# Optimization experiments

Measured on AMD Instinct MI355X. Metric: run time of the kernel, lower is better.

## Reference

```python
import jax, jax.numpy as jnp
import numpy as np

N_NODES = 100000
N_EDGES = 1600000
D = 128

def setup_inputs() -> dict:
    key = jax.random.key(0)
    ks = jax.random.split(key, 8)
    s = 1.0 / np.sqrt(D)
    x = jax.random.normal(ks[0], (N_NODES, D), dtype=jnp.float32)
    edge_index = jax.random.randint(ks[1], (2, N_EDGES), 0, N_NODES, dtype=jnp.int64)
    Wl1 = jax.random.normal(ks[2], (D, D), dtype=jnp.float32) * s
    Wr1 = jax.random.normal(ks[3], (D, D), dtype=jnp.float32) * s
    b1 = jax.random.normal(ks[4], (D,), dtype=jnp.float32) * s
    Wl2 = jax.random.normal(ks[5], (D, D), dtype=jnp.float32) * s
    Wr2 = jax.random.normal(ks[6], (D, D), dtype=jnp.float32) * s
    b2 = jax.random.normal(ks[7], (D,), dtype=jnp.float32) * s
    return {"x": x, "edge_index": edge_index, "Wl1": Wl1, "Wr1": Wr1, "b1": b1,
            "Wl2": Wl2, "Wr2": Wr2, "b2": b2}

def _sage_mean(x, src, dst, n, Wl, Wr, b):
    # mean-aggregate neighbor features onto destination nodes
    msg = x[src]                                      # [E, D] gather
    agg = jax.ops.segment_sum(msg, dst, num_segments=n)  # [N, D] scatter-add
    deg = jax.ops.segment_sum(jnp.ones((src.shape[0],), x.dtype), dst, num_segments=n)
    mean = agg / jnp.maximum(deg, 1.0)[:, None]
    # SAGEConv: lin_l(aggregated) + lin_r(self), bias on lin_l
    return mean @ Wl.T + x @ Wr.T + b

def reference(x, edge_index, Wl1, Wr1, b1, Wl2, Wr2, b2):
    src, dst = edge_index[0], edge_index[1]
    n = x.shape[0]
    h = _sage_mean(x, src, dst, n, Wl1, Wr1, b1)
    h = jax.nn.relu(h)
    return _sage_mean(h, src, dst, n, Wl2, Wr2, b2)
```

## Files before the change

### kernel.cpp

```cpp
#include <hip/hip_runtime.h>
#include <hip/hip_bf16.h>

#define NN 100000
#define NE 1600000
#define DD 128

#define ASHIFT 8
#define NSPAN  256
#define BK     391
#define BCAP   4608
#define EPB    4096
#define NAB    391
#define TFB    3125

typedef __attribute__((ext_vector_type(8))) short bf16x8;
typedef __attribute__((ext_vector_type(4))) float f32x4;
typedef __attribute__((ext_vector_type(2))) float f32x2;

__device__ inline unsigned short f2bf(float f) {
    unsigned u = __builtin_bit_cast(unsigned, f);
    u += 0x7fff + ((u >> 16) & 1);
    return (unsigned short)(u >> 16);
}
__device__ inline float bf2f(unsigned short h) {
    return __builtin_bit_cast(float, (unsigned)h << 16);
}

__global__ __launch_bounds__(512) void fusedA(const int* __restrict__ src,
                                              const int* __restrict__ dst,
                                              int* __restrict__ gcur,
                                              int* __restrict__ pairs,
                                              const float* __restrict__ in,
                                              unsigned short* __restrict__ outb,
                                              unsigned char* __restrict__ out8) {
    __shared__ int hist[BK];
    __shared__ int gbase[BK];
    __shared__ int lcur[BK];
    const int t = threadIdx.x;

    if (blockIdx.x >= NAB) {
        const size_t i = (size_t)(blockIdx.x - NAB) * 512 + t;
        const float4 a = *(const float4*)&in[i * 8];
        const float4 b = *(const float4*)&in[i * 8 + 4];
        unsigned short o[8] = {f2bf(a.x), f2bf(a.y), f2bf(a.z), f2bf(a.w),
                               f2bf(b.x), f2bf(b.y), f2bf(b.z), f2bf(b.w)};
        *(bf16x8*)&outb[i * 8] = *(bf16x8*)o;
        unsigned e0 = 0, e1 = 0;
        e0 = __builtin_amdgcn_cvt_pk_fp8_f32(a.x, a.y, e0, false);
        e0 = __builtin_amdgcn_cvt_pk_fp8_f32(a.z, a.w, e0, true);
        e1 = __builtin_amdgcn_cvt_pk_fp8_f32(b.x, b.y, e1, false);
        e1 = __builtin_amdgcn_cvt_pk_fp8_f32(b.z, b.w, e1, true);
        uint2 p = {e0, e1};
        *(uint2*)&out8[i * 8] = p;
        return;
    }

    const int e0 = blockIdx.x * EPB;

    for (int i = t; i < BK; i += 512) hist[i] = 0;
    __syncthreads();
    for (int i = t; i < EPB; i += 512) {
        int e = e0 + i;
        if (e < NE) atomicAdd(&hist[dst[e] >> ASHIFT], 1);
    }
    __syncthreads();
    for (int i = t; i < BK; i += 512) {
        int c = hist[i];
        gbase[i] = i * BCAP + (c ? atomicAdd(&gcur[i], c) : 0);
        lcur[i] = 0;
    }
    __syncthreads();
    for (int i = t; i < EPB; i += 512) {
        int e = e0 + i;
        if (e < NE) {
            int d = dst[e];
            int b = d >> ASHIFT;
            int r = atomicAdd(&lcur[b], 1);
            pairs[gbase[b] + r] = ((d & (NSPAN - 1)) << 17) | src[e];
        }
    }
}

__global__ __launch_bounds__(512) void bucketB(const int* __restrict__ pairs,
                                               const int* __restrict__ gcur,
                                               int* __restrict__ cnt,
                                               int* __restrict__ rowoff,
                                               int* __restrict__ csr) {
    __shared__ int bs[512];
    __shared__ int hist[NSPAN];
    __shared__ int scanbuf[NSPAN];
    const int b = blockIdx.x, t = threadIdx.x;

    int v = (t < BK) ? gcur[t] : 0;
    bs[t] = v;
    __syncthreads();
    #pragma unroll
    for (int d = 1; d < 512; d <<= 1) {
        int u = (t >= d) ? bs[t - d] : 0;
        __syncthreads();
        bs[t] += u;
        __syncthreads();
    }
    const int sz   = gcur[b];
    const int base = bs[b] - sz;

    const int n0    = b << ASHIFT;
    const int nodeN = min(NSPAN, NN - n0);
    const int* ep   = &pairs[(size_t)b * BCAP];

    for (int i = t; i < NSPAN; i += 512) hist[i] = 0;
    __syncthreads();
    for (int i = t; i < sz; i += 512) atomicAdd(&hist[((unsigned)ep[i]) >> 17], 1);
    __syncthreads();
    for (int i = t; i < nodeN; i += 512) cnt[n0 + i] = hist[i];
    for (int i = t; i < NSPAN; i += 512) scanbuf[i] = hist[i];
    __syncthreads();
    #pragma unroll
    for (int d = 1; d < NSPAN; d <<= 1) {
        int v0 = (t >= d && t < NSPAN) ? scanbuf[t - d] : 0;
        __syncthreads();
        if (t < NSPAN) scanbuf[t] += v0;
        __syncthreads();
    }
    for (int i = t; i < NSPAN; i += 512) {
        int excl = scanbuf[i] - hist[i];
        if (i < nodeN) rowoff[n0 + i] = base + excl;
        hist[i] = excl;
    }
    if (b == BK - 1 && t == 0) rowoff[NN] = NE;
    __syncthreads();
    for (int i = t; i < sz; i += 512) {
        int p = ep[i];
        int r = atomicAdd(&hist[((unsigned)p) >> 17], 1);
        csr[base + r] = p & 0x1FFFF;
    }
}

__global__ __launch_bounds__(256) void prepw(const float* __restrict__ Wl1,
                                             const float* __restrict__ Wr1,
                                             const float* __restrict__ Wl2,
                                             const float* __restrict__ Wr2,
                                             unsigned short* __restrict__ wsb) {
    const int tid = blockIdx.x * 256 + threadIdx.x;
    const int mat = tid >> 11;
    const int ko  = (tid >> 7) & 15;
    const int j   = tid & 127;
    const float* W = (mat == 0) ? Wl1 : (mat == 1) ? Wr1 : (mat == 2) ? Wl2 : Wr2;
    const float4 w0 = *(const float4*)&W[(size_t)j * DD + ko * 8];
    const float4 w1 = *(const float4*)&W[(size_t)j * DD + ko * 8 + 4];
    unsigned short o[8] = {f2bf(w0.x), f2bf(w0.y), f2bf(w0.z), f2bf(w0.w),
                           f2bf(w1.x), f2bf(w1.y), f2bf(w1.z), f2bf(w1.w)};
    *(bf16x8*)&wsb[(size_t)tid * 8] = *(bf16x8*)o;
}

__device__ inline void accum8(float* a, uint2 u) {
    f32x2 p;
    p = __builtin_amdgcn_cvt_pk_f32_fp8(u.x, false); a[0] += p.x; a[1] += p.y;
    p = __builtin_amdgcn_cvt_pk_f32_fp8(u.x, true);  a[2] += p.x; a[3] += p.y;
    p = __builtin_amdgcn_cvt_pk_f32_fp8(u.y, false); a[4] += p.x; a[5] += p.y;
    p = __builtin_amdgcn_cvt_pk_f32_fp8(u.y, true);  a[6] += p.x; a[7] += p.y;
}

__global__ __launch_bounds__(256) void gather_fp8(const unsigned char* __restrict__ feat,
                                                  const int* __restrict__ rowoff,
                                                  const int* __restrict__ csr,
                                                  const int* __restrict__ cnt,
                                                  unsigned short* __restrict__ mean) {
    const int node = blockIdx.x * 16 + (threadIdx.x >> 4);
    const int l8 = (threadIdx.x & 15) * 8;
    const int beg = rowoff[node], end = rowoff[node + 1];
    float a0[8] = {0, 0, 0, 0, 0, 0, 0, 0};
    float a1[8] = {0, 0, 0, 0, 0, 0, 0, 0};
    int j = beg;
    for (; j + 7 < end; j += 8) {
        int s0 = csr[j],     s1 = csr[j + 1], s2 = csr[j + 2], s3 = csr[j + 3];
        int s4 = csr[j + 4], s5 = csr[j + 5], s6 = csr[j + 6], s7 = csr[j + 7];
        uint2 u0 = *(const uint2*)&feat[(size_t)s0 * DD + l8];
        uint2 u1 = *(const uint2*)&feat[(size_t)s1 * DD + l8];
        uint2 u2 = *(const uint2*)&feat[(size_t)s2 * DD + l8];
        uint2 u3 = *(const uint2*)&feat[(size_t)s3 * DD + l8];
        uint2 u4 = *(const uint2*)&feat[(size_t)s4 * DD + l8];
        uint2 u5 = *(const uint2*)&feat[(size_t)s5 * DD + l8];
        uint2 u6 = *(const uint2*)&feat[(size_t)s6 * DD + l8];
        uint2 u7 = *(const uint2*)&feat[(size_t)s7 * DD + l8];
        accum8(a0, u0); accum8(a1, u1); accum8(a0, u2); accum8(a1, u3);
        accum8(a0, u4); accum8(a1, u5); accum8(a0, u6); accum8(a1, u7);
    }
    for (; j + 3 < end; j += 4) {
        int s0 = csr[j], s1 = csr[j + 1], s2 = csr[j + 2], s3 = csr[j + 3];
        uint2 u0 = *(const uint2*)&feat[(size_t)s0 * DD + l8];
        uint2 u1 = *(const uint2*)&feat[(size_t)s1 * DD + l8];
        uint2 u2 = *(const uint2*)&feat[(size_t)s2 * DD + l8];
        uint2 u3 = *(const uint2*)&feat[(size_t)s3 * DD + l8];
        accum8(a0, u0); accum8(a1, u1); accum8(a0, u2); accum8(a1, u3);
    }
    for (; j < end; ++j) {
        int s0 = csr[j];
        uint2 u0 = *(const uint2*)&feat[(size_t)s0 * DD + l8];
        accum8(a0, u0);
    }
    const float inv = 1.0f / fmaxf((float)cnt[node], 1.0f);
    unsigned short o[8];
    #pragma unroll
    for (int i = 0; i < 8; ++i) o[i] = f2bf((a0[i] + a1[i]) * inv);
    *(bf16x8*)&mean[(size_t)node * DD + l8] = *(bf16x8*)o;
}

__global__ __launch_bounds__(256, 3) void combine_mfma(
    const unsigned short* __restrict__ mean, const unsigned short* __restrict__ self,
    const unsigned short* __restrict__ wsb,
    const float* __restrict__ bias, void* __restrict__ outp,
    unsigned char* __restrict__ out8,
    int out_bf16, int do_relu)
{
    const int t = threadIdx.x;
    const int wv = t >> 6, lane = t & 63;
    const int m = lane & 15;
    const int q = lane >> 4;
    const int j0 = wv * 2;

    bf16x8 bfr[2][4][2];
    #pragma unroll
    for (int h = 0; h < 2; ++h)
        #pragma unroll
        for (int kq = 0; kq < 4; ++kq)
            #pragma unroll
            for (int jj = 0; jj < 2; ++jj)
                bfr[h][kq][jj] = *(const bf16x8*)
                    &wsb[((size_t)((h * 16 + kq * 4 + q) * 128) + (j0 + jj) * 16 + m) * 8];

    float bv[2];
    #pragma unroll
    for (int jj = 0; jj < 2; ++jj) bv[jj] = bias[(j0 + jj) * 16 + m];

    for (int tile = blockIdx.x; tile < NN / 16; tile += gridDim.x) {
        const size_t arow = ((size_t)tile * 16 + m) * DD;
        f32x4 acc[2];
        acc[0] = (f32x4){0.f, 0.f, 0.f, 0.f};
        acc[1] = (f32x4){0.f, 0.f, 0.f, 0.f};

        #pragma unroll
        for (int kq = 0; kq < 4; ++kq) {
            const bf16x8 am = *(const bf16x8*)&mean[arow + kq * 32 + q * 8];
            const bf16x8 as = *(const bf16x8*)&self[arow + kq * 32 + q * 8];
            #pragma unroll
            for (int jj = 0; jj < 2; ++jj) {
                acc[jj] = __builtin_amdgcn_mfma_f32_16x16x32_bf16(am, bfr[0][kq][jj], acc[jj], 0, 0, 0);
                acc[jj] = __builtin_amdgcn_mfma_f32_16x16x32_bf16(as, bfr[1][kq][jj], acc[jj], 0, 0, 0);
            }
        }

        #pragma unroll
        for (int jj = 0; jj < 2; ++jj) {
            const int col = (j0 + jj) * 16 + m;
            #pragma unroll
            for (int r = 0; r < 4; ++r) {
                const size_t row = (size_t)tile * 16 + q * 4 + r;
                float v = acc[jj][r] + bv[jj];
                if (do_relu) v = fmaxf(v, 0.0f);
                if (out_bf16)
                    ((unsigned short*)outp)[row * DD + col] = f2bf(v);
                else
                    ((float*)outp)[row * DD + col] = v;
                if (out8) {
                    unsigned p = __builtin_amdgcn_cvt_pk_fp8_f32(v, v, 0u, false);
                    out8[row * DD + col] = (unsigned char)p;
                }
            }
        }
    }
}

extern "C" void kernel_launch(void* const* d_in, const int* in_sizes, int n_in,
                              void* d_out, int out_size, void* d_ws, size_t ws_size,
                              hipStream_t stream) {
    const float* x   = (const float*)d_in[0];
    const int*   ei  = (const int*)d_in[1];
    const float* Wl1 = (const float*)d_in[2];
    const float* Wr1 = (const float*)d_in[3];
    const float* b1  = (const float*)d_in[4];
    const float* Wl2 = (const float*)d_in[5];
    const float* Wr2 = (const float*)d_in[6];
    const float* b2  = (const float*)d_in[7];
    const int* src = ei;
    const int* dst = ei + NE;
    float* out = (float*)d_out;

    unsigned short* xb   = (unsigned short*)d_ws;
    unsigned short* mean = xb + (size_t)NN * DD;
    unsigned short* h    = mean + (size_t)NN * DD;
    unsigned char*  x8   = (unsigned char*)(h + (size_t)NN * DD);
    unsigned char*  h8   = x8 + (size_t)NN * DD;
    int*  pairs  = (int*)(h8 + (size_t)NN * DD);
    int*  gcur   = pairs + (size_t)BK * BCAP;
    int*  cnt    = gcur + BK;
    int*  rowoff = cnt + NN;
    int*  csr    = rowoff + NN + 1;
    uintptr_t wp = ((uintptr_t)(csr + NE) + 255) & ~(uintptr_t)255;
    unsigned short* wsb = (unsigned short*)wp;

    hipMemsetAsync(gcur, 0, BK * sizeof(int), stream);
    prepw<<<32, 256, 0, stream>>>(Wl1, Wr1, Wl2, Wr2, wsb);
    fusedA<<<NAB + TFB, 512, 0, stream>>>(src, dst, gcur, pairs, x, xb, x8);
    bucketB<<<BK, 512, 0, stream>>>(pairs, gcur, cnt, rowoff, csr);

    gather_fp8<<<NN / 16, 256, 0, stream>>>(x8, rowoff, csr, cnt, mean);
    combine_mfma<<<2048, 256, 0, stream>>>(mean, xb, wsb, b1, h, h8, 1, 1);

    gather_fp8<<<NN / 16, 256, 0, stream>>>(h8, rowoff, csr, cnt, mean);
    combine_mfma<<<2048, 256, 0, stream>>>(mean, h, wsb + 32768, b2, out, nullptr, 0, 0);
}
```

Measured before the change: 289.5 us.

## Replace two-pass bucketed CSR build with global-atomic degree count and scatter

Drops the bucket-then-sort CSR construction, which staged edges through a pairs buffer and ran a local per-bucket sort. It is replaced by three passes: global atomic degree counting (fused with the bf16/fp8 conversion of x), a per-block scan that claims its base offset from a global atomic counter, and a scatter that places each edge using global atomics. Node segments no longer follow node order because block bases are taken in arrival order, so gather now uses rowoff plus cnt instead of rowoff[n+1]. This removes the pairs buffer traffic at the cost of heavy global atomic contention and a CSR order that is no longer deterministic.

```diff
diff --git a/kernel.cpp b/kernel.cpp
--- a/kernel.cpp
+++ b/kernel.cpp
@@ -5,13 +5,10 @@
 #define NE 1600000
 #define DD 128
 
-#define ASHIFT 8
-#define NSPAN  256
-#define BK     391
-#define BCAP   4608
-#define EPB    4096
-#define NAB    391
-#define TFB    3125
+#define DEGB 782
+#define TFB  3125
+#define SCT  782
+#define MKB  196
 
 typedef __attribute__((ext_vector_type(8))) short bf16x8;
 typedef __attribute__((ext_vector_type(4))) float f32x4;
@@ -26,20 +23,15 @@
     return __builtin_bit_cast(float, (unsigned)h << 16);
 }
 
-__global__ __launch_bounds__(512) void fusedA(const int* __restrict__ src,
-                                              const int* __restrict__ dst,
-                                              int* __restrict__ gcur,
-                                              int* __restrict__ pairs,
-                                              const float* __restrict__ in,
-                                              unsigned short* __restrict__ outb,
-                                              unsigned char* __restrict__ out8) {
-    __shared__ int hist[BK];
-    __shared__ int gbase[BK];
-    __shared__ int lcur[BK];
+__global__ __launch_bounds__(512) void fusedAdeg(const int* __restrict__ dst,
+                                                 int* __restrict__ cnt,
+                                                 const float* __restrict__ in,
+                                                 unsigned short* __restrict__ outb,
+                                                 unsigned char* __restrict__ out8) {
     const int t = threadIdx.x;
 
-    if (blockIdx.x >= NAB) {
-        const size_t i = (size_t)(blockIdx.x - NAB) * 512 + t;
+    if (blockIdx.x >= DEGB) {
+        const size_t i = (size_t)(blockIdx.x - DEGB) * 512 + t;
         const float4 a = *(const float4*)&in[i * 8];
         const float4 b = *(const float4*)&in[i * 8 + 4];
         unsigned short o[8] = {f2bf(a.x), f2bf(a.y), f2bf(a.z), f2bf(a.w),
@@ -55,43 +47,29 @@
         return;
     }
 
-    const int e0 = blockIdx.x * EPB;
-
-    for (int i = t; i < BK; i += 512) hist[i] = 0;
-    __syncthreads();
-    for (int i = t; i < EPB; i += 512) {
-        int e = e0 + i;
-        if (e < NE) atomicAdd(&hist[dst[e] >> ASHIFT], 1);
-    }
-    __syncthreads();
-    for (int i = t; i < BK; i += 512) {
-        int c = hist[i];
-        gbase[i] = i * BCAP + (c ? atomicAdd(&gcur[i], c) : 0);
-        lcur[i] = 0;
-    }
-    __syncthreads();
-    for (int i = t; i < EPB; i += 512) {
-        int e = e0 + i;
-        if (e < NE) {
-            int d = dst[e];
-            int b = d >> ASHIFT;
-            int r = atomicAdd(&lcur[b], 1);
-            pairs[gbase[b] + r] = ((d & (NSPAN - 1)) << 17) | src[e];
-        }
-    }
-}
-
-__global__ __launch_bounds__(512) void bucketB(const int* __restrict__ pairs,
-                                               const int* __restrict__ gcur,
-                                               int* __restrict__ cnt,
-                                               int* __restrict__ rowoff,
-                                               int* __restrict__ csr) {
+    const int gid = blockIdx.x * 512 + t;
+    const int ST  = DEGB * 512;
+    const int e0 = gid, e1 = gid + ST, e2 = gid + 2 * ST, e3 = gid + 3 * ST;
+    int d0 = dst[e0];
+    int d1 = dst[e1];
+    int d2 = dst[e2];
+    const bool v3 = e3 < NE;
+    int d3 = v3 ? dst[e3] : 0;
+    atomicAdd(&cnt[d0], 1);
+    atomicAdd(&cnt[d1], 1);
+    atomicAdd(&cnt[d2], 1);
+    if (v3) atomicAdd(&cnt[d3], 1);
+}
+
+__global__ __launch_bounds__(512) void mkoff(const int* __restrict__ cnt,
+                                             int* __restrict__ gctr,
+                                             int* __restrict__ rowoff,
+                                             int* __restrict__ cur) {
     __shared__ int bs[512];
-    __shared__ int hist[NSPAN];
-    __shared__ int scanbuf[NSPAN];
-    const int b = blockIdx.x, t = threadIdx.x;
-
-    int v = (t < BK) ? gcur[t] : 0;
+    __shared__ int baseb;
+    const int t = threadIdx.x;
+    const int n = blockIdx.x * 512 + t;
+    const int v = (n < NN) ? cnt[n] : 0;
     bs[t] = v;
     __syncthreads();
     #pragma unroll
@@ -101,39 +79,35 @@
         bs[t] += u;
         __syncthreads();
     }
-    const int sz   = gcur[b];
-    const int base = bs[b] - sz;
-
-    const int n0    = b << ASHIFT;
-    const int nodeN = min(NSPAN, NN - n0);
-    const int* ep   = &pairs[(size_t)b * BCAP];
-
-    for (int i = t; i < NSPAN; i += 512) hist[i] = 0;
+    if (t == 511) baseb = atomicAdd(gctr, bs[511]);
     __syncthreads();
-    for (int i = t; i < sz; i += 512) atomicAdd(&hist[((unsigned)ep[i]) >> 17], 1);
-    __syncthreads();
-    for (int i = t; i < nodeN; i += 512) cnt[n0 + i] = hist[i];
-    for (int i = t; i < NSPAN; i += 512) scanbuf[i] = hist[i];
-    __syncthreads();
-    #pragma unroll
-    for (int d = 1; d < NSPAN; d <<= 1) {
-        int v0 = (t >= d && t < NSPAN) ? scanbuf[t - d] : 0;
-        __syncthreads();
-        if (t < NSPAN) scanbuf[t] += v0;
-        __syncthreads();
-    }
-    for (int i = t; i < NSPAN; i += 512) {
-        int excl = scanbuf[i] - hist[i];
-        if (i < nodeN) rowoff[n0 + i] = base + excl;
-        hist[i] = excl;
-    }
-    if (b == BK - 1 && t == 0) rowoff[NN] = NE;
-    __syncthreads();
-    for (int i = t; i < sz; i += 512) {
-        int p = ep[i];
-        int r = atomicAdd(&hist[((unsigned)p) >> 17], 1);
-        csr[base + r] = p & 0x1FFFF;
-    }
+    if (n < NN) {
+        const int off = baseb + bs[t] - v;
+        rowoff[n] = off;
+        cur[n] = off;
+    }
+}
+
+__global__ __launch_bounds__(512) void scatter(const int* __restrict__ src,
+                                               const int* __restrict__ dst,
+                                               int* __restrict__ cur,
+                                               int* __restrict__ csr) {
+    const int gid = blockIdx.x * 512 + threadIdx.x;
+    const int ST  = SCT * 512;
+    const int e0 = gid, e1 = gid + ST, e2 = gid + 2 * ST, e3 = gid + 3 * ST;
+    int d0 = dst[e0], s0 = src[e0];
+    int d1 = dst[e1], s1 = src[e1];
+    int d2 = dst[e2], s2 = src[e2];
+    const bool v3 = e3 < NE;
+    int d3 = v3 ? dst[e3] : 0, s3 = v3 ? src[e3] : 0;
+    int r0 = atomicAdd(&cur[d0], 1);
+    int r1 = atomicAdd(&cur[d1], 1);
+    int r2 = atomicAdd(&cur[d2], 1);
+    int r3 = v3 ? atomicAdd(&cur[d3], 1) : 0;
+    csr[r0] = s0;
+    csr[r1] = s1;
+    csr[r2] = s2;
+    if (v3) csr[r3] = s3;
 }
 
 __global__ __launch_bounds__(256) void prepw(const float* __restrict__ Wl1,
@@ -168,7 +142,9 @@
                                                   unsigned short* __restrict__ mean) {
     const int node = blockIdx.x * 16 + (threadIdx.x >> 4);
     const int l8 = (threadIdx.x & 15) * 8;
-    const int beg = rowoff[node], end = rowoff[node + 1];
+    const int beg = rowoff[node];
+    const int deg = cnt[node];
+    const int end = beg + deg;
     float a0[8] = {0, 0, 0, 0, 0, 0, 0, 0};
     float a1[8] = {0, 0, 0, 0, 0, 0, 0, 0};
     int j = beg;
@@ -199,7 +175,7 @@
         uint2 u0 = *(const uint2*)&feat[(size_t)s0 * DD + l8];
         accum8(a0, u0);
     }
-    const float inv = 1.0f / fmaxf((float)cnt[node], 1.0f);
+    const float inv = 1.0f / fmaxf((float)deg, 1.0f);
     unsigned short o[8];
     #pragma unroll
     for (int i = 0; i < 8; ++i) o[i] = f2bf((a0[i] + a1[i]) * inv);
@@ -291,18 +267,19 @@
     unsigned short* h    = mean + (size_t)NN * DD;
     unsigned char*  x8   = (unsigned char*)(h + (size_t)NN * DD);
     unsigned char*  h8   = x8 + (size_t)NN * DD;
-    int*  pairs  = (int*)(h8 + (size_t)NN * DD);
-    int*  gcur   = pairs + (size_t)BK * BCAP;
-    int*  cnt    = gcur + BK;
-    int*  rowoff = cnt + NN;
-    int*  csr    = rowoff + NN + 1;
+    int*  cnt    = (int*)(h8 + (size_t)NN * DD);
+    int*  gctr   = cnt + NN;
+    int*  cur    = gctr + 1;
+    int*  rowoff = cur + NN;
+    int*  csr    = rowoff + NN;
     uintptr_t wp = ((uintptr_t)(csr + NE) + 255) & ~(uintptr_t)255;
     unsigned short* wsb = (unsigned short*)wp;
 
-    hipMemsetAsync(gcur, 0, BK * sizeof(int), stream);
+    hipMemsetAsync(cnt, 0, (NN + 1) * sizeof(int), stream);
     prepw<<<32, 256, 0, stream>>>(Wl1, Wr1, Wl2, Wr2, wsb);
-    fusedA<<<NAB + TFB, 512, 0, stream>>>(src, dst, gcur, pairs, x, xb, x8);
-    bucketB<<<BK, 512, 0, stream>>>(pairs, gcur, cnt, rowoff, csr);
+    fusedAdeg<<<DEGB + TFB, 512, 0, stream>>>(dst, cnt, x, xb, x8);
+    mkoff<<<MKB, 512, 0, stream>>>(cnt, gctr, rowoff, cur);
+    scatter<<<SCT, 512, 0, stream>>>(src, dst, cur, csr);
 
     gather_fp8<<<NN / 16, 256, 0, stream>>>(x8, rowoff, csr, cnt, mean);
     combine_mfma<<<2048, 256, 0, stream>>>(mean, xb, wsb, b1, h, h8, 1, 1);
```

Measured after the change: 443.5 us. +53.2%, slower.

## Fold weight prep into bucketing kernel and split feature conversion across two kernels

Applied to the files above, without the earlier changes.

Removes the separate prepw launch by adding weight-conversion blocks to the first bucketing kernel. The x-to-bf16/fp8 conversion is split in half, with one half run alongside edge bucketing and the other alongside CSR building, to balance the two launches. Edge bucketing now handles 8192 edges per block and caches the dst indices in registers so they are not read twice. This cuts one launch and overlaps conversion with latency-bound bucketing work, at the cost of higher register use per thread and fewer bucketing blocks.

```diff
diff --git a/kernel.cpp b/kernel.cpp
--- a/kernel.cpp
+++ b/kernel.cpp
@@ -9,9 +9,11 @@
 #define NSPAN  256
 #define BK     391
 #define BCAP   4608
-#define EPB    4096
-#define NAB    391
-#define TFB    3125
+#define EPB    8192
+#define NAB    196
+#define TFH    1563
+#define HELEM  800000
+#define PWB    16
 
 typedef __attribute__((ext_vector_type(8))) short bf16x8;
 typedef __attribute__((ext_vector_type(4))) float f32x4;
@@ -26,43 +28,75 @@
     return __builtin_bit_cast(float, (unsigned)h << 16);
 }
 
-__global__ __launch_bounds__(512) void fusedA(const int* __restrict__ src,
-                                              const int* __restrict__ dst,
-                                              int* __restrict__ gcur,
-                                              int* __restrict__ pairs,
-                                              const float* __restrict__ in,
-                                              unsigned short* __restrict__ outb,
-                                              unsigned char* __restrict__ out8) {
+__device__ inline void tofeat_body(int half, int blk, int t,
+                                   const float* __restrict__ in,
+                                   unsigned short* __restrict__ outb,
+                                   unsigned char* __restrict__ out8) {
+    const size_t local = (size_t)blk * 512 + t;
+    if (local >= HELEM) return;
+    const size_t i = (size_t)half * HELEM + local;
+    const float4 a = *(const float4*)&in[i * 8];
+    const float4 b = *(const float4*)&in[i * 8 + 4];
+    unsigned short o[8] = {f2bf(a.x), f2bf(a.y), f2bf(a.z), f2bf(a.w),
+                           f2bf(b.x), f2bf(b.y), f2bf(b.z), f2bf(b.w)};
+    *(bf16x8*)&outb[i * 8] = *(bf16x8*)o;
+    unsigned e0 = 0, e1 = 0;
+    e0 = __builtin_amdgcn_cvt_pk_fp8_f32(a.x, a.y, e0, false);
+    e0 = __builtin_amdgcn_cvt_pk_fp8_f32(a.z, a.w, e0, true);
+    e1 = __builtin_amdgcn_cvt_pk_fp8_f32(b.x, b.y, e1, false);
+    e1 = __builtin_amdgcn_cvt_pk_fp8_f32(b.z, b.w, e1, true);
+    uint2 p = {e0, e1};
+    *(uint2*)&out8[i * 8] = p;
+}
+
+__global__ __launch_bounds__(512) void fusedA2(const int* __restrict__ src,
+                                               const int* __restrict__ dst,
+                                               int* __restrict__ gcur,
+                                               int* __restrict__ pairs,
+                                               const float* __restrict__ in,
+                                               unsigned short* __restrict__ outb,
+                                               unsigned char* __restrict__ out8,
+                                               const float* __restrict__ Wl1,
+                                               const float* __restrict__ Wr1,
+                                               const float* __restrict__ Wl2,
+                                               const float* __restrict__ Wr2,
+                                               unsigned short* __restrict__ wsb) {
     __shared__ int hist[BK];
     __shared__ int gbase[BK];
     __shared__ int lcur[BK];
     const int t = threadIdx.x;
 
+    if (blockIdx.x >= NAB + TFH) {
+        const int tid = (blockIdx.x - NAB - TFH) * 512 + t;
+        const int mat = tid >> 11;
+        const int ko  = (tid >> 7) & 15;
+        const int j   = tid & 127;
+        const float* W = (mat == 0) ? Wl1 : (mat == 1) ? Wr1 : (mat == 2) ? Wl2 : Wr2;
+        const float4 w0 = *(const float4*)&W[(size_t)j * DD + ko * 8];
+        const float4 w1 = *(const float4*)&W[(size_t)j * DD + ko * 8 + 4];
+        unsigned short o[8] = {f2bf(w0.x), f2bf(w0.y), f2bf(w0.z), f2bf(w0.w),
+                               f2bf(w1.x), f2bf(w1.y), f2bf(w1.z), f2bf(w1.w)};
+        *(bf16x8*)&wsb[(size_t)tid * 8] = *(bf16x8*)o;
+        return;
+    }
     if (blockIdx.x >= NAB) {
-        const size_t i = (size_t)(blockIdx.x - NAB) * 512 + t;
-        const float4 a = *(const float4*)&in[i * 8];
-        const float4 b = *(const float4*)&in[i * 8 + 4];
-        unsigned short o[8] = {f2bf(a.x), f2bf(a.y), f2bf(a.z), f2bf(a.w),
-                               f2bf(b.x), f2bf(b.y), f2bf(b.z), f2bf(b.w)};
-        *(bf16x8*)&outb[i * 8] = *(bf16x8*)o;
-        unsigned e0 = 0, e1 = 0;
-        e0 = __builtin_amdgcn_cvt_pk_fp8_f32(a.x, a.y, e0, false);
-        e0 = __builtin_amdgcn_cvt_pk_fp8_f32(a.z, a.w, e0, true);
-        e1 = __builtin_amdgcn_cvt_pk_fp8_f32(b.x, b.y, e1, false);
-        e1 = __builtin_amdgcn_cvt_pk_fp8_f32(b.z, b.w, e1, true);
-        uint2 p = {e0, e1};
-        *(uint2*)&out8[i * 8] = p;
+        tofeat_body(0, blockIdx.x - NAB, t, in, outb, out8);
         return;
     }
 
     const int e0 = blockIdx.x * EPB;
+    int dcache[16];
+    #pragma unroll
+    for (int k = 0; k < 16; ++k) {
+        const int e = e0 + t + k * 512;
+        dcache[k] = (e < NE) ? dst[e] : -1;
+    }
 
     for (int i = t; i < BK; i += 512) hist[i] = 0;
     __syncthreads();
-    for (int i = t; i < EPB; i += 512) {
-        int e = e0 + i;
-        if (e < NE) atomicAdd(&hist[dst[e] >> ASHIFT], 1);
-    }
+    #pragma unroll
+    for (int k = 0; k < 16; ++k)
+        if (dcache[k] >= 0) atomicAdd(&hist[dcache[k] >> ASHIFT], 1);
     __syncthreads();
     for (int i = t; i < BK; i += 512) {
         int c = hist[i];
@@ -70,27 +104,37 @@
         lcur[i] = 0;
     }
     __syncthreads();
-    for (int i = t; i < EPB; i += 512) {
-        int e = e0 + i;
-        if (e < NE) {
-            int d = dst[e];
-            int b = d >> ASHIFT;
-            int r = atomicAdd(&lcur[b], 1);
+    #pragma unroll
+    for (int k = 0; k < 16; ++k) {
+        const int e = e0 + t + k * 512;
+        const int d = dcache[k];
+        if (d >= 0) {
+            const int b = d >> ASHIFT;
+            const int r = atomicAdd(&lcur[b], 1);
             pairs[gbase[b] + r] = ((d & (NSPAN - 1)) << 17) | src[e];
         }
     }
 }
 
-__global__ __launch_bounds__(512) void bucketB(const int* __restrict__ pairs,
+__global__ __launch_bounds__(512) void fusedB2(const int* __restrict__ pairs,
                                                const int* __restrict__ gcur,
                                                int* __restrict__ cnt,
                                                int* __restrict__ rowoff,
-                                               int* __restrict__ csr) {
+                                               int* __restrict__ csr,
+                                               const float* __restrict__ in,
+                                               unsigned short* __restrict__ outb,
+                                               unsigned char* __restrict__ out8) {
     __shared__ int bs[512];
     __shared__ int hist[NSPAN];
     __shared__ int scanbuf[NSPAN];
-    const int b = blockIdx.x, t = threadIdx.x;
-
+    const int t = threadIdx.x;
+
+    if (blockIdx.x >= BK) {
+        tofeat_body(1, blockIdx.x - BK, t, in, outb, out8);
+        return;
+    }
+
+    const int b = blockIdx.x;
     int v = (t < BK) ? gcur[t] : 0;
     bs[t] = v;
     __syncthreads();
@@ -134,23 +178,6 @@
         int r = atomicAdd(&hist[((unsigned)p) >> 17], 1);
         csr[base + r] = p & 0x1FFFF;
     }
-}
-
-__global__ __launch_bounds__(256) void prepw(const float* __restrict__ Wl1,
-                                             const float* __restrict__ Wr1,
-                                             const float* __restrict__ Wl2,
-                                             const float* __restrict__ Wr2,
-                                             unsigned short* __restrict__ wsb) {
-    const int tid = blockIdx.x * 256 + threadIdx.x;
-    const int mat = tid >> 11;
-    const int ko  = (tid >> 7) & 15;
-    const int j   = tid & 127;
-    const float* W = (mat == 0) ? Wl1 : (mat == 1) ? Wr1 : (mat == 2) ? Wl2 : Wr2;
-    const float4 w0 = *(const float4*)&W[(size_t)j * DD + ko * 8];
-    const float4 w1 = *(const float4*)&W[(size_t)j * DD + ko * 8 + 4];
-    unsigned short o[8] = {f2bf(w0.x), f2bf(w0.y), f2bf(w0.z), f2bf(w0.w),
-                           f2bf(w1.x), f2bf(w1.y), f2bf(w1.z), f2bf(w1.w)};
-    *(bf16x8*)&wsb[(size_t)tid * 8] = *(bf16x8*)o;
 }
 
 __device__ inline void accum8(float* a, uint2 u) {
@@ -300,9 +327,10 @@
     unsigned short* wsb = (unsigned short*)wp;
 
     hipMemsetAsync(gcur, 0, BK * sizeof(int), stream);
-    prepw<<<32, 256, 0, stream>>>(Wl1, Wr1, Wl2, Wr2, wsb);
-    fusedA<<<NAB + TFB, 512, 0, stream>>>(src, dst, gcur, pairs, x, xb, x8);
-    bucketB<<<BK, 512, 0, stream>>>(pairs, gcur, cnt, rowoff, csr);
+    fusedA2<<<NAB + TFH + PWB, 512, 0, stream>>>(src, dst, gcur, pairs,
+                                                 x, xb, x8,
+                                                 Wl1, Wr1, Wl2, Wr2, wsb);
+    fusedB2<<<BK + TFH, 512, 0, stream>>>(pairs, gcur, cnt, rowoff, csr, x, xb, x8);
 
     gather_fp8<<<NN / 16, 256, 0, stream>>>(x8, rowoff, csr, cnt, mean);
     combine_mfma<<<2048, 256, 0, stream>>>(mean, xb, wsb, b1, h, h8, 1, 1);
```

Result: faster. 279.4 us (-3.5%).
